# Optimization experiments

Measured on AMD Instinct MI355X. Metric: run time of the kernel, lower is better.

Reference implementation:

```python
import jax, jax.numpy as jnp
import numpy as np

N_NODES = 100000
N_EDGES = 3200000
N_GRAPHS = 1000
NODE_DIM = 16
EDGE_DIM = 16


def setup_inputs() -> dict:
    key = jax.random.key(0)
    ks = jax.random.split(key, 12)
    edge_index = jax.random.randint(ks[0], (2, N_EDGES), 0, N_NODES, dtype=jnp.int64)
    node_attr = jax.random.normal(ks[1], (N_NODES, NODE_DIM), dtype=jnp.float32)
    edge_attr = jax.random.normal(ks[2], (N_EDGES, EDGE_DIM), dtype=jnp.float32)
    batch = jnp.sort(jax.random.randint(ks[3], (N_NODES,), 0, N_GRAPHS, dtype=jnp.int64))
    def lin(k, fan_in, fan_out):
        k1, k2 = jax.random.split(k)
        bound = 1.0 / np.sqrt(fan_in)
        W = jax.random.uniform(k1, (fan_in, fan_out), minval=-bound, maxval=bound, dtype=jnp.float32)
        b = jax.random.uniform(k2, (fan_out,), minval=-bound, maxval=bound, dtype=jnp.float32)
        return W, b
    W_mpl, b_mpl = lin(ks[4], NODE_DIM + EDGE_DIM, 10)
    W1, b1 = lin(ks[5], 10, 10)
    W2, b2 = lin(ks[6], 10, 5)
    W3, b3 = lin(ks[7], 5, 5)
    W4, b4 = lin(ks[8], 5, 1)
    return {
        'edge_index': edge_index, 'node_attr': node_attr, 'edge_attr': edge_attr, 'batch': batch,
        'W_mpl': W_mpl, 'b_mpl': b_mpl, 'W1': W1, 'b1': b1, 'W2': W2, 'b2': b2,
        'W3': W3, 'b3': b3, 'W4': W4, 'b4': b4,
    }


def reference(edge_index, node_attr, edge_attr, batch,
              W_mpl, b_mpl, W1, b1, W2, b2, W3, b3, W4, b4):
    src, dst = edge_index[0], edge_index[1]
    # MPL_1: per-edge message from gathered source node feats + edge feats
    msg_in = jnp.concatenate([node_attr[src], edge_attr], axis=-1)  # [E, 32]
    msg = jnp.tanh(msg_in @ W_mpl + b_mpl)                          # [E, 10]
    x = jax.ops.segment_sum(msg, dst, num_segments=N_NODES)        # [N, 10]
    # tiny MLP chain on nodes
    x = jnp.tanh(x @ W1 + b1)   # [N, 10]
    x = jnp.tanh(x @ W2 + b2)   # [N, 5]
    # per-graph sum pooling (segment_coo with reduce='sum')
    g = jax.ops.segment_sum(x, batch, num_segments=N_GRAPHS)       # [G, 5]
    g = jnp.tanh(g @ W3 + b3)   # [G, 5]
    return g @ W4 + b4          # [G, 1]
```

## Files before the change

### kernel.cpp

```cpp
#include <hip/hip_runtime.h>

#define N_NODES  100000
#define N_EDGES  3200000
#define N_GRAPHS 1000

#define NPB      128
#define NB       782
#define CAPL     4608

typedef float    f32x4 __attribute__((ext_vector_type(4)));
typedef unsigned u32x4 __attribute__((ext_vector_type(4)));

#define HIST_OFF   0
#define BASE_OFF   4096
#define CUR_OFF    8192
#define G_OFF      12288
#define ZERO_BYTES 32768
#define P_OFF      32768
#define ENT_OFF    4832768
#define WS_FAT     (ENT_OFF + (size_t)N_EDGES * 32)

#define S_T      1024
#define S_GRID   512
#define S_E      6250
#define S_K      7
#define BK_T     1024

#define L_CAP      4500
#define L_OVF_CAP  16384
#define L_BLK_E    8192
#define L_S1_GRID  ((N_EDGES + L_BLK_E - 1) / L_BLK_E)
#define L_CUR_OFF    0
#define L_OVFC_OFF   4096
#define L_G_OFF      4352
#define L_ZERO_BYTES 24576
#define L_OVF_OFF    24576
#define L_SORT_OFF   163840
#define L_WS_NEED    (L_SORT_OFF + (size_t)NB * L_CAP * 8)

__device__ __forceinline__ float fast_tanh(float x) {
    float e = __expf(2.0f * x);
    return 1.0f - 2.0f * __builtin_amdgcn_rcpf(e + 1.0f);
}

__device__ __forceinline__ unsigned pkh(float a, float b) {
    union { _Float16 h[2]; unsigned u; } c;
    c.h[0] = (_Float16)a; c.h[1] = (_Float16)b;
    return c.u;
}
__device__ __forceinline__ void upkh(unsigned u, float& a, float& b) {
    union { unsigned u; _Float16 h[2]; } c;
    c.u = u;
    a = (float)c.h[0]; b = (float)c.h[1];
}


__global__ __launch_bounds__(1024) void hist_kernel(
    const int* __restrict__ ei, unsigned* __restrict__ hist)
{
    __shared__ unsigned lh[NB];
    const int tid = threadIdx.x;
    for (int b = tid; b < NB; b += 1024) lh[b] = 0u;
    __syncthreads();
    for (int e = blockIdx.x * 1024 + tid; e < N_EDGES; e += gridDim.x * 1024) {
        int d = __builtin_nontemporal_load(ei + N_EDGES + e);
        atomicAdd(&lh[d >> 7], 1u);
    }
    __syncthreads();
    for (int b = tid; b < NB; b += 1024)
        if (lh[b]) atomicAdd(hist + b, lh[b]);
}

__global__ __launch_bounds__(1024) void scan_kernel(
    const unsigned* __restrict__ hist,
    unsigned* __restrict__ base, unsigned* __restrict__ cursor)
{
    __shared__ unsigned A[NB];
    const int i = threadIdx.x;
    unsigned h0 = 0;
    if (i < NB) { h0 = hist[i]; A[i] = h0; }
    __syncthreads();
    #pragma unroll
    for (int off = 1; off < NB; off <<= 1) {
        unsigned t = 0;
        if (i < NB && i >= off) t = A[i - off];
        __syncthreads();
        if (i < NB) A[i] += t;
        __syncthreads();
    }
    if (i < NB) {
        unsigned excl = A[i] - h0;
        base[i] = excl;
        cursor[i] = excl;
        if (i == NB - 1) base[NB] = A[i];
    }
}

__global__ __launch_bounds__(256) void nodeproj_kernel(
    const float* __restrict__ node_attr, const float* __restrict__ Wm,
    unsigned* __restrict__ P)
{
    int n = blockIdx.x * 256 + threadIdx.x;
    if (n >= N_NODES) return;
    float r[16];
    const f32x4* na = reinterpret_cast<const f32x4*>(node_attr + (size_t)n * 16);
    #pragma unroll
    for (int q = 0; q < 4; ++q) {
        f32x4 v = na[q];
        r[q*4+0] = v.x; r[q*4+1] = v.y; r[q*4+2] = v.z; r[q*4+3] = v.w;
    }
    float p[10];
    #pragma unroll
    for (int j = 0; j < 10; ++j) p[j] = 0.0f;
    #pragma unroll
    for (int i = 0; i < 16; ++i) {
        float xi = r[i];
        #pragma unroll
        for (int j = 0; j < 10; ++j) p[j] = fmaf(xi, Wm[i*10 + j], p[j]);
    }
    u32x4* pd = reinterpret_cast<u32x4*>(P + (size_t)n * 8);
    u32x4 w0 = {pkh(p[0],p[1]), pkh(p[2],p[3]), pkh(p[4],p[5]), pkh(p[6],p[7])};
    u32x4 w1 = {pkh(p[8],p[9]), 0u, 0u, 0u};
    pd[0] = w0; pd[1] = w1;
}

__global__ __launch_bounds__(S_T, 4) void scatter_msg_kernel(
    const int* __restrict__ ei, const float* __restrict__ edge_attr,
    const unsigned* __restrict__ P,
    const float* __restrict__ Wm, const float* __restrict__ bm,
    unsigned* __restrict__ cursor, unsigned* __restrict__ entries)
{
    __shared__ unsigned lh[NB];
    __shared__ unsigned lb[NB];
    const int tid  = threadIdx.x;
    const int e0   = blockIdx.x * S_E;
    const int e1   = e0 + S_E;
    const int last = e1 - 1;

    for (int b = tid; b < NB; b += S_T) lh[b] = 0u;
    __syncthreads();

    int dch[S_K];
    unsigned rch[S_K];
    #pragma unroll
    for (int k = 0; k < S_K; ++k) {
        int e = e0 + k * S_T + tid;
        int d = (e < e1) ? __builtin_nontemporal_load(ei + N_EDGES + e) : -1;
        dch[k] = d;
        rch[k] = (d >= 0) ? atomicAdd(&lh[d >> 7], 1u) : 0u;
    }
    __syncthreads();

    for (int b = tid; b < NB; b += S_T) {
        unsigned c = lh[b];
        lb[b] = c ? atomicAdd(cursor + b, c) : 0u;
    }
    __syncthreads();

    unsigned mch[S_K];
    #pragma unroll
    for (int k = 0; k < S_K; ++k) {
        int d = dch[k];
        mch[k] = (d >= 0) ? (((lb[d >> 7] + rch[k]) << 7) | (unsigned)(d & 127))
                          : 0xFFFFFFFFu;
    }

    const int eBase = e0 + tid;
    #define ECL(x) ((x) > last ? last : (x))

    int sA = __builtin_nontemporal_load(ei + ECL(eBase));
    int sB = __builtin_nontemporal_load(ei + ECL(eBase + S_T));
    f32x4 rA0, rA1, rA2, rA3;
    {
        const f32x4* ea = reinterpret_cast<const f32x4*>(edge_attr + (size_t)ECL(eBase) * 16);
        rA0 = __builtin_nontemporal_load(ea + 0);
        rA1 = __builtin_nontemporal_load(ea + 1);
        rA2 = __builtin_nontemporal_load(ea + 2);
        rA3 = __builtin_nontemporal_load(ea + 3);
    }
    u32x4 pA; unsigned pA4;
    {
        const u32x4* pp = reinterpret_cast<const u32x4*>(P + (size_t)sA * 8);
        pA = pp[0]; pA4 = P[(size_t)sA * 8 + 4];
    }

    #pragma unroll
    for (int k = 0; k < S_K; ++k) {
        const int e = eBase + k * S_T;

        int sC = 0;
        if (k + 2 < S_K) sC = __builtin_nontemporal_load(ei + ECL(e + 2 * S_T));

        f32x4 rB0 = rA0, rB1 = rA1, rB2 = rA2, rB3 = rA3;
        if (k + 1 < S_K) {
            const f32x4* ea = reinterpret_cast<const f32x4*>(edge_attr + (size_t)ECL(e + S_T) * 16);
            rB0 = __builtin_nontemporal_load(ea + 0);
            rB1 = __builtin_nontemporal_load(ea + 1);
            rB2 = __builtin_nontemporal_load(ea + 2);
            rB3 = __builtin_nontemporal_load(ea + 3);
        }
        u32x4 pB = pA; unsigned pB4 = pA4;
        if (k + 1 < S_K) {
            const u32x4* pp = reinterpret_cast<const u32x4*>(P + (size_t)sB * 8);
            pB = pp[0]; pB4 = P[(size_t)sB * 8 + 4];
        }

        const unsigned mc = mch[k];
        if (mc != 0xFFFFFFFFu) {
            float r[16];
            r[0]=rA0.x; r[1]=rA0.y; r[2]=rA0.z; r[3]=rA0.w;
            r[4]=rA1.x; r[5]=rA1.y; r[6]=rA1.z; r[7]=rA1.w;
            r[8]=rA2.x; r[9]=rA2.y; r[10]=rA2.z; r[11]=rA2.w;
            r[12]=rA3.x; r[13]=rA3.y; r[14]=rA3.z; r[15]=rA3.w;

            float B[10];
            #pragma unroll
            for (int j = 0; j < 10; ++j) B[j] = bm[j];
            #pragma unroll
            for (int i = 0; i < 16; ++i) {
                float xi = r[i];
                #pragma unroll
                for (int j = 0; j < 10; ++j) B[j] = fmaf(xi, Wm[(16 + i)*10 + j], B[j]);
            }
            float Pv[10];
            upkh(pA.x, Pv[0], Pv[1]);
            upkh(pA.y, Pv[2], Pv[3]);
            upkh(pA.z, Pv[4], Pv[5]);
            upkh(pA.w, Pv[6], Pv[7]);
            upkh(pA4,  Pv[8], Pv[9]);
            float m[10];
            #pragma unroll
            for (int j = 0; j < 10; ++j) m[j] = fast_tanh(B[j] + Pv[j]);

            unsigned pos = mc >> 7;
            u32x4* ep = reinterpret_cast<u32x4*>(entries + (size_t)pos * 8);
            u32x4 w0 = {pkh(m[0],m[1]), pkh(m[2],m[3]), pkh(m[4],m[5]), pkh(m[6],m[7])};
            u32x4 w1 = {pkh(m[8],m[9]), mc & 127u, 0u, 0u};
            ep[0] = w0;
            ep[1] = w1;
        }

        rA0 = rB0; rA1 = rB1; rA2 = rB2; rA3 = rB3;
        pA = pB; pA4 = pB4;
        sB = sC;
    }
    #undef ECL
}

__global__ __launch_bounds__(BK_T, 8) void bucket_sort_kernel(
    const unsigned* __restrict__ entries, const unsigned* __restrict__ base,
    const int* __restrict__ batch,
    const float* __restrict__ W1, const float* __restrict__ b1,
    const float* __restrict__ W2, const float* __restrict__ b2,
    float* __restrict__ g)
{
    __shared__ unsigned seq[CAPL];
    __shared__ unsigned ord[CAPL];
    __shared__ unsigned h[NPB], st[NPB], c2[NPB];
    __shared__ float gacc[64][5];
    __shared__ int bse[2];
    const int tid = threadIdx.x;
    const int b   = blockIdx.x;
    const unsigned lo  = base[b];
    const unsigned cnt = min(base[b + 1] - lo, (unsigned)CAPL);

    if (tid < NPB) h[tid] = 0u;
    __syncthreads();

    for (unsigned i = tid; i < cnt; i += BK_T) {
        unsigned dl = entries[(size_t)(lo + i) * 8 + 5] & 127u;
        seq[i] = dl;
        atomicAdd(&h[dl], 1u);
    }
    __syncthreads();

    if (tid < NPB) st[tid] = h[tid];
    __syncthreads();
    #pragma unroll
    for (int off = 1; off < NPB; off <<= 1) {
        unsigned t = 0;
        if (tid < NPB && tid >= off) t = st[tid - off];
        __syncthreads();
        if (tid < NPB) st[tid] += t;
        __syncthreads();
    }
    if (tid < NPB) { unsigned e = st[tid] - h[tid]; st[tid] = e; c2[tid] = e; }
    __syncthreads();

    for (unsigned i = tid; i < cnt; i += BK_T) {
        unsigned pos = atomicAdd(&c2[seq[i]], 1u);
        ord[pos] = i;
    }
    __syncthreads();

    if (tid == 0) {
        int nfirst = b * NPB;
        int nlast  = min(nfirst + NPB - 1, N_NODES - 1);
        bse[0] = batch[nfirst];
        bse[1] = batch[nlast];
    }
    __syncthreads();
    const int bmin = bse[0];
    const int R    = bse[1] - bmin + 1;
    const bool lds_pool = (R <= 64);
    if (lds_pool)
        for (int i = tid; i < R * 5; i += BK_T) ((float*)gacc)[i] = 0.0f;
    __syncthreads();

    const int dl = tid >> 3, s = tid & 7;
    float a[10];
    #pragma unroll
    for (int j = 0; j < 10; ++j) a[j] = 0.0f;
    {
        const unsigned s0 = st[dl], c = h[dl];
        for (unsigned p = s; p < c; p += 8) {
            unsigned li = ord[s0 + p];
            const u32x4* ep = reinterpret_cast<const u32x4*>(entries + (size_t)(lo + li) * 8);
            u32x4 v0 = ep[0];
            u32x4 v1 = ep[1];
            float x0, x1;
            upkh(v0.x, x0, x1); a[0] += x0; a[1] += x1;
            upkh(v0.y, x0, x1); a[2] += x0; a[3] += x1;
            upkh(v0.z, x0, x1); a[4] += x0; a[5] += x1;
            upkh(v0.w, x0, x1); a[6] += x0; a[7] += x1;
            upkh(v1.x, x0, x1); a[8] += x0; a[9] += x1;
        }
    }
    #pragma unroll
    for (int msk = 4; msk >= 1; msk >>= 1) {
        #pragma unroll
        for (int j = 0; j < 10; ++j) a[j] += __shfl_xor(a[j], msk, 64);
    }

    const int n = b * NPB + dl;
    if (s == 0 && n < N_NODES) {
        float h1[10];
        #pragma unroll
        for (int j = 0; j < 10; ++j) h1[j] = b1[j];
        #pragma unroll
        for (int i = 0; i < 10; ++i) {
            float xi = a[i];
            #pragma unroll
            for (int j = 0; j < 10; ++j) h1[j] = fmaf(xi, W1[i*10 + j], h1[j]);
        }
        #pragma unroll
        for (int j = 0; j < 10; ++j) h1[j] = fast_tanh(h1[j]);

        float h2[5];
        #pragma unroll
        for (int j = 0; j < 5; ++j) h2[j] = b2[j];
        #pragma unroll
        for (int i = 0; i < 10; ++i) {
            float xi = h1[i];
            #pragma unroll
            for (int j = 0; j < 5; ++j) h2[j] = fmaf(xi, W2[i*5 + j], h2[j]);
        }

        const int bg = batch[n];
        if (lds_pool) {
            #pragma unroll
            for (int j = 0; j < 5; ++j) atomicAdd(&gacc[bg - bmin][j], fast_tanh(h2[j]));
        } else {
            #pragma unroll
            for (int j = 0; j < 5; ++j) atomicAdd(g + (size_t)bg * 5 + j, fast_tanh(h2[j]));
        }
    }
    __syncthreads();

    if (lds_pool) {
        for (int i = tid; i < R * 5; i += BK_T) {
            float v = ((float*)gacc)[i];
            if (v != 0.0f) atomicAdd(g + (size_t)bmin * 5 + i, v);
        }
    }
}

__global__ __launch_bounds__(256) void graph_kernel(
    const float* __restrict__ g,
    const float* __restrict__ W3, const float* __restrict__ b3,
    const float* __restrict__ W4, const float* __restrict__ b4,
    float* __restrict__ out)
{
    int i = blockIdx.x * 256 + threadIdx.x;
    if (i >= N_GRAPHS) return;
    float t[5];
    #pragma unroll
    for (int j = 0; j < 5; ++j) t[j] = b3[j];
    #pragma unroll
    for (int k = 0; k < 5; ++k) {
        float gk = g[(size_t)i * 5 + k];
        #pragma unroll
        for (int j = 0; j < 5; ++j) t[j] = fmaf(gk, W3[k*5 + j], t[j]);
    }
    float o = b4[0];
    #pragma unroll
    for (int k = 0; k < 5; ++k) o = fmaf(fast_tanh(t[k]), W4[k], o);
    out[i] = o;
}

__global__ __launch_bounds__(1024) void scatter_legacy_kernel(
    const int* __restrict__ ei, uint2* __restrict__ sorted,
    unsigned* __restrict__ cursor, unsigned* __restrict__ ovf_cnt,
    uint2* __restrict__ ovf)
{
    __shared__ unsigned hist[NB];
    __shared__ unsigned lbase[NB];
    const int tid = threadIdx.x;
    const int e0  = blockIdx.x * L_BLK_E;

    for (int b = tid; b < NB; b += 1024) hist[b] = 0u;
    __syncthreads();

    int dcache[L_BLK_E / 1024];
    #pragma unroll
    for (int k = 0; k < L_BLK_E / 1024; ++k) {
        int e = e0 + k * 1024 + tid;
        int d = (e < N_EDGES) ? __builtin_nontemporal_load(ei + N_EDGES + e) : -1;
        dcache[k] = d;
        if (d >= 0) atomicAdd(&hist[d >> 7], 1u);
    }
    __syncthreads();
    for (int b = tid; b < NB; b += 1024) {
        unsigned c = hist[b];
        lbase[b] = c ? atomicAdd(cursor + b, c) : 0u;
        hist[b] = 0u;
    }
    __syncthreads();
    #pragma unroll
    for (int k = 0; k < L_BLK_E / 1024; ++k) {
        int d = dcache[k];
        if (d < 0) continue;
        int e = e0 + k * 1024 + tid;
        int s = __builtin_nontemporal_load(ei + e);
        int bk = d >> 7;
        unsigned pos = lbase[bk] + atomicAdd(&hist[bk], 1u);
        uint2 ent;
        ent.x = (unsigned)e | ((unsigned)bk << 22);
        ent.y = (unsigned)s | ((unsigned)(d & 127) << 17);
        if (pos < L_CAP) sorted[(size_t)bk * L_CAP + pos] = ent;
        else {
            unsigned op = atomicAdd(ovf_cnt, 1u);
            if (op < L_OVF_CAP) ovf[op] = ent;
        }
    }
}

__device__ __forceinline__ void legacy_accum_edge(
    uint2 ent, const float* __restrict__ node_attr, const float* __restrict__ edge_attr,
    const float* __restrict__ Wm, const float* __restrict__ bm, float (*acc)[10])
{
    unsigned eid = ent.x & 0x3FFFFFu;
    unsigned src = ent.y & 0x1FFFFu;
    unsigned dl  = (ent.y >> 17) & 0x7Fu;
    float in[32];
    const f32x4* na = reinterpret_cast<const f32x4*>(node_attr + (size_t)src * 16);
    const f32x4* ea = reinterpret_cast<const f32x4*>(edge_attr + (size_t)eid * 16);
    #pragma unroll
    for (int q = 0; q < 4; ++q) { f32x4 v = na[q];
        in[q*4]=v.x; in[q*4+1]=v.y; in[q*4+2]=v.z; in[q*4+3]=v.w; }
    #pragma unroll
    for (int q = 0; q < 4; ++q) { f32x4 v = __builtin_nontemporal_load(ea + q);
        in[16+q*4]=v.x; in[16+q*4+1]=v.y; in[16+q*4+2]=v.z; in[16+q*4+3]=v.w; }
    float m[10];
    #pragma unroll
    for (int j = 0; j < 10; ++j) m[j] = bm[j];
    #pragma unroll
    for (int i = 0; i < 32; ++i) {
        float xi = in[i];
        #pragma unroll
        for (int j = 0; j < 10; ++j) m[j] = fmaf(xi, Wm[i*10 + j], m[j]);
    }
    #pragma unroll
    for (int j = 0; j < 10; ++j) atomicAdd(&acc[dl][j], fast_tanh(m[j]));
}

__global__ __launch_bounds__(1024, 8) void bucket_legacy_kernel(
    const uint2* __restrict__ sorted, const unsigned* __restrict__ cursor,
    const unsigned* __restrict__ ovf_cnt, const uint2* __restrict__ ovf,
    const float* __restrict__ node_attr, const float* __restrict__ edge_attr,
    const int* __restrict__ batch,
    const float* __restrict__ Wm, const float* __restrict__ bm,
    const float* __restrict__ W1, const float* __restrict__ b1,
    const float* __restrict__ W2, const float* __restrict__ b2,
    float* __restrict__ g)
{
    __shared__ float acc[NPB][10];
    __shared__ float gacc[64][5];
    __shared__ int bse[2];
    const int tid = threadIdx.x;
    const int b   = blockIdx.x;

    for (int i = tid; i < NPB * 10; i += 1024) ((float*)acc)[i] = 0.0f;
    __syncthreads();

    const unsigned cnt = min(cursor[b], (unsigned)L_CAP);
    const uint2* basep = sorted + (size_t)b * L_CAP;
    for (unsigned i = tid; i < cnt; i += 1024)
        legacy_accum_edge(basep[i], node_attr, edge_attr, Wm, bm, acc);
    __syncthreads();

    unsigned L = min(*ovf_cnt, (unsigned)L_OVF_CAP);
    if (L) {
        for (unsigned i = tid; i < L; i += 1024) {
            uint2 ent = ovf[i];
            if ((ent.x >> 22) == (unsigned)b)
                legacy_accum_edge(ent, node_attr, edge_attr, Wm, bm, acc);
        }
        __syncthreads();
    }

    if (tid == 0) {
        int nfirst = b * NPB;
        int nlast  = min(nfirst + NPB - 1, N_NODES - 1);
        bse[0] = batch[nfirst]; bse[1] = batch[nlast];
    }
    __syncthreads();
    const int bmin = bse[0];
    const int R    = bse[1] - bse[0] + 1;
    const bool lds_pool = (R <= 64);
    if (lds_pool)
        for (int i = tid; i < R * 5; i += 1024) ((float*)gacc)[i] = 0.0f;
    __syncthreads();

    const int n = b * NPB + tid;
    if (tid < NPB && n < N_NODES) {
        float h1[10];
        #pragma unroll
        for (int j = 0; j < 10; ++j) h1[j] = b1[j];
        #pragma unroll
        for (int i = 0; i < 10; ++i) {
            float xi = acc[tid][i];
            #pragma unroll
            for (int j = 0; j < 10; ++j) h1[j] = fmaf(xi, W1[i*10 + j], h1[j]);
        }
        #pragma unroll
        for (int j = 0; j < 10; ++j) h1[j] = fast_tanh(h1[j]);
        float h2[5];
        #pragma unroll
        for (int j = 0; j < 5; ++j) h2[j] = b2[j];
        #pragma unroll
        for (int i = 0; i < 10; ++i) {
            float xi = h1[i];
            #pragma unroll
            for (int j = 0; j < 5; ++j) h2[j] = fmaf(xi, W2[i*5 + j], h2[j]);
        }
        const int bg = batch[n];
        if (lds_pool) {
            #pragma unroll
            for (int j = 0; j < 5; ++j) atomicAdd(&gacc[bg - bmin][j], fast_tanh(h2[j]));
        } else {
            #pragma unroll
            for (int j = 0; j < 5; ++j) atomicAdd(g + (size_t)bg * 5 + j, fast_tanh(h2[j]));
        }
    }
    __syncthreads();
    if (lds_pool) {
        for (int i = tid; i < R * 5; i += 1024) {
            float v = ((float*)gacc)[i];
            if (v != 0.0f) atomicAdd(g + (size_t)bmin * 5 + i, v);
        }
    }
}

extern "C" void kernel_launch(void* const* d_in, const int* in_sizes, int n_in,
                              void* d_out, int out_size, void* d_ws, size_t ws_size,
                              hipStream_t stream) {
    const int*   ei        = (const int*)  d_in[0];
    const float* node_attr = (const float*)d_in[1];
    const float* edge_attr = (const float*)d_in[2];
    const int*   batch     = (const int*)  d_in[3];
    const float* Wm = (const float*)d_in[4];
    const float* bm = (const float*)d_in[5];
    const float* W1 = (const float*)d_in[6];
    const float* b1 = (const float*)d_in[7];
    const float* W2 = (const float*)d_in[8];
    const float* b2 = (const float*)d_in[9];
    const float* W3 = (const float*)d_in[10];
    const float* b3 = (const float*)d_in[11];
    const float* W4 = (const float*)d_in[12];
    const float* b4 = (const float*)d_in[13];
    float* out = (float*)d_out;
    char* ws = (char*)d_ws;

    if (ws_size >= WS_FAT) {
        unsigned* hist   = (unsigned*)(ws + HIST_OFF);
        unsigned* base   = (unsigned*)(ws + BASE_OFF);
        unsigned* cursor = (unsigned*)(ws + CUR_OFF);
        float*    g      = (float*)   (ws + G_OFF);
        unsigned* P      = (unsigned*)(ws + P_OFF);
        unsigned* ent    = (unsigned*)(ws + ENT_OFF);

        (void)hipMemsetAsync(ws, 0, ZERO_BYTES, stream);
        hist_kernel<<<256, 1024, 0, stream>>>(ei, hist);
        nodeproj_kernel<<<(N_NODES + 255) / 256, 256, 0, stream>>>(node_attr, Wm, P);
        scan_kernel<<<1, 1024, 0, stream>>>(hist, base, cursor);
        scatter_msg_kernel<<<S_GRID, S_T, 0, stream>>>(ei, edge_attr, P, Wm, bm, cursor, ent);
        bucket_sort_kernel<<<NB, BK_T, 0, stream>>>(ent, base, batch, W1, b1, W2, b2, g);
        graph_kernel<<<(N_GRAPHS + 255) / 256, 256, 0, stream>>>(g, W3, b3, W4, b4, out);
    } else if (ws_size >= L_WS_NEED) {
        unsigned* cursor  = (unsigned*)(ws + L_CUR_OFF);
        unsigned* ovf_cnt = (unsigned*)(ws + L_OVFC_OFF);
        float*    g       = (float*)   (ws + L_G_OFF);
        uint2*    ovf     = (uint2*)   (ws + L_OVF_OFF);
        uint2*    sorted  = (uint2*)   (ws + L_SORT_OFF);

        (void)hipMemsetAsync(ws, 0, L_ZERO_BYTES, stream);
        scatter_legacy_kernel<<<L_S1_GRID, 1024, 0, stream>>>(ei, sorted, cursor, ovf_cnt, ovf);
        bucket_legacy_kernel<<<NB, 1024, 0, stream>>>(sorted, cursor, ovf_cnt, ovf,
                                                      node_attr, edge_attr, batch,
                                                      Wm, bm, W1, b1, W2, b2, g);
        graph_kernel<<<(N_GRAPHS + 255) / 256, 256, 0, stream>>>(g, W3, b3, W4, b4, out);
    }
}
```

Before: 243.8 us.

## Replace histogram+scan with fixed-capacity buckets and global overflow list

Removes the separate histogram and prefix-scan kernels by giving each destination bucket a fixed capacity slot region, so the scatter kernel takes offsets directly from a per-bucket cursor starting at zero. Entries that exceed the capacity go to a global overflow buffer, which every bucket block scans linearly and merges. Source indices are now loaded up front alongside destinations so the node projection prefetch is two steps ahead. This saves one full pass over the destination indices and two launches, at the cost of a per-block overflow scan and a larger, sparser entry buffer.

```diff
diff --git a/kernel.cpp b/kernel.cpp
--- a/kernel.cpp
+++ b/kernel.cpp
@@ -7,18 +7,19 @@
 #define NPB      128
 #define NB       782
 #define CAPL     4608
+#define OVF_CAP  16384
 
 typedef float    f32x4 __attribute__((ext_vector_type(4)));
 typedef unsigned u32x4 __attribute__((ext_vector_type(4)));
 
-#define HIST_OFF   0
-#define BASE_OFF   4096
-#define CUR_OFF    8192
-#define G_OFF      12288
-#define ZERO_BYTES 32768
-#define P_OFF      32768
-#define ENT_OFF    4832768
-#define WS_FAT     (ENT_OFF + (size_t)N_EDGES * 32)
+#define CUR_OFF    0
+#define OVFC_OFF   4096
+#define G_OFF      4352
+#define ZERO_BYTES 24576
+#define OVF_OFF    24576
+#define P_OFF      548864
+#define ENT_OFF    3748864
+#define WS_FAT     (ENT_OFF + (size_t)NB * CAPL * 32)
 
 #define S_T      1024
 #define S_GRID   512
@@ -55,47 +56,6 @@
 }
 
 
-__global__ __launch_bounds__(1024) void hist_kernel(
-    const int* __restrict__ ei, unsigned* __restrict__ hist)
-{
-    __shared__ unsigned lh[NB];
-    const int tid = threadIdx.x;
-    for (int b = tid; b < NB; b += 1024) lh[b] = 0u;
-    __syncthreads();
-    for (int e = blockIdx.x * 1024 + tid; e < N_EDGES; e += gridDim.x * 1024) {
-        int d = __builtin_nontemporal_load(ei + N_EDGES + e);
-        atomicAdd(&lh[d >> 7], 1u);
-    }
-    __syncthreads();
-    for (int b = tid; b < NB; b += 1024)
-        if (lh[b]) atomicAdd(hist + b, lh[b]);
-}
-
-__global__ __launch_bounds__(1024) void scan_kernel(
-    const unsigned* __restrict__ hist,
-    unsigned* __restrict__ base, unsigned* __restrict__ cursor)
-{
-    __shared__ unsigned A[NB];
-    const int i = threadIdx.x;
-    unsigned h0 = 0;
-    if (i < NB) { h0 = hist[i]; A[i] = h0; }
-    __syncthreads();
-    #pragma unroll
-    for (int off = 1; off < NB; off <<= 1) {
-        unsigned t = 0;
-        if (i < NB && i >= off) t = A[i - off];
-        __syncthreads();
-        if (i < NB) A[i] += t;
-        __syncthreads();
-    }
-    if (i < NB) {
-        unsigned excl = A[i] - h0;
-        base[i] = excl;
-        cursor[i] = excl;
-        if (i == NB - 1) base[NB] = A[i];
-    }
-}
-
 __global__ __launch_bounds__(256) void nodeproj_kernel(
     const float* __restrict__ node_attr, const float* __restrict__ Wm,
     unsigned* __restrict__ P)
@@ -128,26 +88,30 @@
     const int* __restrict__ ei, const float* __restrict__ edge_attr,
     const unsigned* __restrict__ P,
     const float* __restrict__ Wm, const float* __restrict__ bm,
-    unsigned* __restrict__ cursor, unsigned* __restrict__ entries)
+    unsigned* __restrict__ cursor, unsigned* __restrict__ entries,
+    unsigned* __restrict__ ovf_cnt, unsigned* __restrict__ ovf)
 {
     __shared__ unsigned lh[NB];
     __shared__ unsigned lb[NB];
-    const int tid  = threadIdx.x;
-    const int e0   = blockIdx.x * S_E;
-    const int e1   = e0 + S_E;
-    const int last = e1 - 1;
+    const int tid = threadIdx.x;
+    const int e0  = blockIdx.x * S_E;
+    const int e1  = e0 + S_E;
 
     for (int b = tid; b < NB; b += S_T) lh[b] = 0u;
     __syncthreads();
 
-    int dch[S_K];
+    int dch[S_K], sch[S_K];
     unsigned rch[S_K];
     #pragma unroll
     for (int k = 0; k < S_K; ++k) {
         int e = e0 + k * S_T + tid;
-        int d = (e < e1) ? __builtin_nontemporal_load(ei + N_EDGES + e) : -1;
-        dch[k] = d;
-        rch[k] = (d >= 0) ? atomicAdd(&lh[d >> 7], 1u) : 0u;
+        bool v = (e < e1);
+        int ec = v ? e : (e1 - 1);
+        int d = __builtin_nontemporal_load(ei + N_EDGES + ec);
+        int s = __builtin_nontemporal_load(ei + ec);
+        dch[k] = v ? d : -1;
+        sch[k] = s;
+        rch[k] = v ? atomicAdd(&lh[d >> 7], 1u) : 0u;
     }
     __syncthreads();
 
@@ -161,15 +125,20 @@
     #pragma unroll
     for (int k = 0; k < S_K; ++k) {
         int d = dch[k];
-        mch[k] = (d >= 0) ? (((lb[d >> 7] + rch[k]) << 7) | (unsigned)(d & 127))
-                          : 0xFFFFFFFFu;
+        if (d >= 0) {
+            unsigned bk = (unsigned)(d >> 7);
+            unsigned pl = lb[bk] + rch[k];
+            mch[k] = (pl < CAPL) ? ((((unsigned)bk * CAPL + pl) << 7) | (unsigned)(d & 127))
+                                 : (0x80000000u | (bk << 7) | (unsigned)(d & 127));
+        } else {
+            mch[k] = 0xFFFFFFFFu;
+        }
     }
 
     const int eBase = e0 + tid;
+    const int last  = e1 - 1;
     #define ECL(x) ((x) > last ? last : (x))
 
-    int sA = __builtin_nontemporal_load(ei + ECL(eBase));
-    int sB = __builtin_nontemporal_load(ei + ECL(eBase + S_T));
     f32x4 rA0, rA1, rA2, rA3;
     {
         const f32x4* ea = reinterpret_cast<const f32x4*>(edge_attr + (size_t)ECL(eBase) * 16);
@@ -180,16 +149,18 @@
     }
     u32x4 pA; unsigned pA4;
     {
-        const u32x4* pp = reinterpret_cast<const u32x4*>(P + (size_t)sA * 8);
-        pA = pp[0]; pA4 = P[(size_t)sA * 8 + 4];
+        const u32x4* pp = reinterpret_cast<const u32x4*>(P + (size_t)sch[0] * 8);
+        pA = pp[0]; pA4 = P[(size_t)sch[0] * 8 + 4];
+    }
+    u32x4 pB; unsigned pB4;
+    {
+        const u32x4* pp = reinterpret_cast<const u32x4*>(P + (size_t)sch[1] * 8);
+        pB = pp[0]; pB4 = P[(size_t)sch[1] * 8 + 4];
     }
 
     #pragma unroll
     for (int k = 0; k < S_K; ++k) {
         const int e = eBase + k * S_T;
-
-        int sC = 0;
-        if (k + 2 < S_K) sC = __builtin_nontemporal_load(ei + ECL(e + 2 * S_T));
 
         f32x4 rB0 = rA0, rB1 = rA1, rB2 = rA2, rB3 = rA3;
         if (k + 1 < S_K) {
@@ -199,10 +170,10 @@
             rB2 = __builtin_nontemporal_load(ea + 2);
             rB3 = __builtin_nontemporal_load(ea + 3);
         }
-        u32x4 pB = pA; unsigned pB4 = pA4;
-        if (k + 1 < S_K) {
-            const u32x4* pp = reinterpret_cast<const u32x4*>(P + (size_t)sB * 8);
-            pB = pp[0]; pB4 = P[(size_t)sB * 8 + 4];
+        u32x4 pC = pB; unsigned pC4 = pB4;
+        if (k + 2 < S_K) {
+            const u32x4* pp = reinterpret_cast<const u32x4*>(P + (size_t)sch[k + 2] * 8);
+            pC = pp[0]; pC4 = P[(size_t)sch[k + 2] * 8 + 4];
         }
 
         const unsigned mc = mch[k];
@@ -232,23 +203,34 @@
             #pragma unroll
             for (int j = 0; j < 10; ++j) m[j] = fast_tanh(B[j] + Pv[j]);
 
-            unsigned pos = mc >> 7;
-            u32x4* ep = reinterpret_cast<u32x4*>(entries + (size_t)pos * 8);
             u32x4 w0 = {pkh(m[0],m[1]), pkh(m[2],m[3]), pkh(m[4],m[5]), pkh(m[6],m[7])};
-            u32x4 w1 = {pkh(m[8],m[9]), mc & 127u, 0u, 0u};
-            ep[0] = w0;
-            ep[1] = w1;
+            if (!(mc & 0x80000000u)) {
+                unsigned pos = mc >> 7;
+                u32x4* ep = reinterpret_cast<u32x4*>(entries + (size_t)pos * 8);
+                u32x4 w1 = {pkh(m[8],m[9]), mc & 127u, 0u, 0u};
+                ep[0] = w0;
+                ep[1] = w1;
+            } else {
+                unsigned op = atomicAdd(ovf_cnt, 1u);
+                if (op < OVF_CAP) {
+                    u32x4* ep = reinterpret_cast<u32x4*>(ovf + (size_t)op * 8);
+                    u32x4 w1 = {pkh(m[8],m[9]), mc & 0x7FFFFFFFu, 0u, 0u};
+                    ep[0] = w0;
+                    ep[1] = w1;
+                }
+            }
         }
 
         rA0 = rB0; rA1 = rB1; rA2 = rB2; rA3 = rB3;
         pA = pB; pA4 = pB4;
-        sB = sC;
+        pB = pC; pB4 = pC4;
     }
     #undef ECL
 }
 
 __global__ __launch_bounds__(BK_T, 8) void bucket_sort_kernel(
-    const unsigned* __restrict__ entries, const unsigned* __restrict__ base,
+    const unsigned* __restrict__ entries, const unsigned* __restrict__ cursor,
+    const unsigned* __restrict__ ovf_cnt, const unsigned* __restrict__ ovf,
     const int* __restrict__ batch,
     const float* __restrict__ W1, const float* __restrict__ b1,
     const float* __restrict__ W2, const float* __restrict__ b2,
@@ -261,14 +243,14 @@
     __shared__ int bse[2];
     const int tid = threadIdx.x;
     const int b   = blockIdx.x;
-    const unsigned lo  = base[b];
-    const unsigned cnt = min(base[b + 1] - lo, (unsigned)CAPL);
+    const size_t   lo  = (size_t)b * CAPL;
+    const unsigned cnt = min(cursor[b], (unsigned)CAPL);
 
     if (tid < NPB) h[tid] = 0u;
     __syncthreads();
 
     for (unsigned i = tid; i < cnt; i += BK_T) {
-        unsigned dl = entries[(size_t)(lo + i) * 8 + 5] & 127u;
+        unsigned dl = entries[(lo + i) * 8 + 5] & 127u;
         seq[i] = dl;
         atomicAdd(&h[dl], 1u);
     }
@@ -315,7 +297,7 @@
         const unsigned s0 = st[dl], c = h[dl];
         for (unsigned p = s; p < c; p += 8) {
             unsigned li = ord[s0 + p];
-            const u32x4* ep = reinterpret_cast<const u32x4*>(entries + (size_t)(lo + li) * 8);
+            const u32x4* ep = reinterpret_cast<const u32x4*>(entries + (lo + li) * 8);
             u32x4 v0 = ep[0];
             u32x4 v1 = ep[1];
             float x0, x1;
@@ -330,6 +312,24 @@
     for (int msk = 4; msk >= 1; msk >>= 1) {
         #pragma unroll
         for (int j = 0; j < 10; ++j) a[j] += __shfl_xor(a[j], msk, 64);
+    }
+
+    unsigned L = min(*ovf_cnt, (unsigned)OVF_CAP);
+    if (L) {
+        for (unsigned i = 0; i < L; ++i) {
+            const u32x4* ep = reinterpret_cast<const u32x4*>(ovf + (size_t)i * 8);
+            u32x4 v0 = ep[0];
+            u32x4 v1 = ep[1];
+            unsigned meta = v1.y;
+            if ((int)(meta >> 7) == b && (int)(meta & 127u) == dl && s == 0) {
+                float x0, x1;
+                upkh(v0.x, x0, x1); a[0] += x0; a[1] += x1;
+                upkh(v0.y, x0, x1); a[2] += x0; a[3] += x1;
+                upkh(v0.z, x0, x1); a[4] += x0; a[5] += x1;
+                upkh(v0.w, x0, x1); a[6] += x0; a[7] += x1;
+                upkh(v1.x, x0, x1); a[8] += x0; a[9] += x1;
+            }
+        }
     }
 
     const int n = b * NPB + dl;
@@ -583,19 +583,19 @@
     char* ws = (char*)d_ws;
 
     if (ws_size >= WS_FAT) {
-        unsigned* hist   = (unsigned*)(ws + HIST_OFF);
-        unsigned* base   = (unsigned*)(ws + BASE_OFF);
-        unsigned* cursor = (unsigned*)(ws + CUR_OFF);
-        float*    g      = (float*)   (ws + G_OFF);
-        unsigned* P      = (unsigned*)(ws + P_OFF);
-        unsigned* ent    = (unsigned*)(ws + ENT_OFF);
+        unsigned* cursor  = (unsigned*)(ws + CUR_OFF);
+        unsigned* ovf_cnt = (unsigned*)(ws + OVFC_OFF);
+        float*    g       = (float*)   (ws + G_OFF);
+        unsigned* ovf     = (unsigned*)(ws + OVF_OFF);
+        unsigned* P       = (unsigned*)(ws + P_OFF);
+        unsigned* ent     = (unsigned*)(ws + ENT_OFF);
 
         (void)hipMemsetAsync(ws, 0, ZERO_BYTES, stream);
-        hist_kernel<<<256, 1024, 0, stream>>>(ei, hist);
         nodeproj_kernel<<<(N_NODES + 255) / 256, 256, 0, stream>>>(node_attr, Wm, P);
-        scan_kernel<<<1, 1024, 0, stream>>>(hist, base, cursor);
-        scatter_msg_kernel<<<S_GRID, S_T, 0, stream>>>(ei, edge_attr, P, Wm, bm, cursor, ent);
-        bucket_sort_kernel<<<NB, BK_T, 0, stream>>>(ent, base, batch, W1, b1, W2, b2, g);
+        scatter_msg_kernel<<<S_GRID, S_T, 0, stream>>>(ei, edge_attr, P, Wm, bm,
+                                                       cursor, ent, ovf_cnt, ovf);
+        bucket_sort_kernel<<<NB, BK_T, 0, stream>>>(ent, cursor, ovf_cnt, ovf,
+                                                    batch, W1, b1, W2, b2, g);
         graph_kernel<<<(N_GRAPHS + 255) / 256, 256, 0, stream>>>(g, W3, b3, W4, b4, out);
     } else if (ws_size >= L_WS_NEED) {
         unsigned* cursor  = (unsigned*)(ws + L_CUR_OFF);
```

After: 230.8 us. 5.3% less time.
